# Optimization experiments

Measured on AMD Instinct MI355X. Metric: run time of the kernel, lower is better.

Reference implementation:

```python
import jax, jax.numpy as jnp
import numpy as np

N = 50_000       # nodes
E = 1_600_000    # edges per edge set (avg degree 32)
D = 128          # hidden dim
F_IN = 1273      # fixed num_features in NetGIN
G = 512          # graphs in batch
STEPS = 6        # Set2Set processing steps
BN_EPS = 1e-5


def setup_inputs() -> dict:
    key = jax.random.key(0)
    ks = iter(jax.random.split(key, 40))
    def rn(shape, fan_in):
        return jax.random.normal(next(ks), shape, jnp.float32) / np.float32(np.sqrt(fan_in))
    inp = {}
    inp["x"] = jax.random.normal(next(ks), (N, F_IN), jnp.float32)
    for i in (1, 2, 3):
        inp[f"edge_index_{i}"] = jax.random.randint(next(ks), (2, E), 0, N, jnp.int32)
    inp["batch"] = jnp.sort(jax.random.randint(next(ks), (N,), 0, G, jnp.int32))
    # GINConv MLPs: layer 1 has input F_IN, layers 2-6 have input D
    inp["conv1_W1"] = rn((3, F_IN, D), F_IN)
    inp["conv1_b1"] = jnp.zeros((3, D), jnp.float32)
    inp["conv_rest_W1"] = rn((5, 3, D, D), D)
    inp["conv_rest_b1"] = jnp.zeros((5, 3, D), jnp.float32)
    inp["conv_W2"] = rn((6, 3, D, D), D)
    inp["conv_b2"] = jnp.zeros((6, 3, D), jnp.float32)
    inp["conv_bn1_g"] = jnp.ones((6, 3, D), jnp.float32)
    inp["conv_bn1_b"] = jnp.zeros((6, 3, D), jnp.float32)
    inp["conv_bn2_g"] = jnp.ones((6, 3, D), jnp.float32)
    inp["conv_bn2_b"] = jnp.zeros((6, 3, D), jnp.float32)
    inp["conv_eps"] = jnp.zeros((6, 3), jnp.float32)  # train_eps=True, init 0
    # fusion MLPs (3*D -> D -> D)
    inp["mlp_W1"] = rn((6, 3 * D, D), 3 * D)
    inp["mlp_b1"] = jnp.zeros((6, D), jnp.float32)
    inp["mlp_bn1_g"] = jnp.ones((6, D), jnp.float32)
    inp["mlp_bn1_b"] = jnp.zeros((6, D), jnp.float32)
    inp["mlp_W2"] = rn((6, D, D), D)
    inp["mlp_b2"] = jnp.zeros((6, D), jnp.float32)
    inp["mlp_bn2_g"] = jnp.ones((6, D), jnp.float32)
    inp["mlp_bn2_b"] = jnp.zeros((6, D), jnp.float32)
    # Set2Set single-layer LSTM: input 2D, hidden D; gate order i,f,g,o
    inp["lstm_Wih"] = rn((4 * D, 2 * D), 2 * D)
    inp["lstm_Whh"] = rn((4 * D, D), D)
    inp["lstm_bih"] = jnp.zeros((4 * D,), jnp.float32)
    inp["lstm_bhh"] = jnp.zeros((4 * D,), jnp.float32)
    inp["fc1_W"] = rn((2 * D, D), 2 * D)
    inp["fc1_b"] = jnp.zeros((D,), jnp.float32)
    inp["fc4_W"] = rn((D, 12), D)
    inp["fc4_b"] = jnp.zeros((12,), jnp.float32)
    return inp


def _bn(x, g, b):
    # BatchNorm1d in training mode: batch statistics (biased var), eps=1e-5
    mu = jnp.mean(x, axis=0)
    var = jnp.var(x, axis=0)
    return g * (x - mu) * jax.lax.rsqrt(var + BN_EPS) + b


def _mlp2(h, W1, b1, g1, bb1, W2, b2, g2, bb2):
    h = jax.nn.relu(_bn(h @ W1 + b1, g1, bb1))
    return jax.nn.relu(_bn(h @ W2 + b2, g2, bb2))


def _gin(h, ei, eps, W1, b1, g1, bb1, W2, b2, g2, bb2):
    # sum-aggregate neighbor features: out[dst] += h[src]
    agg = jax.ops.segment_sum(h[ei[0]], ei[1], num_segments=h.shape[0])
    return _mlp2((1.0 + eps) * h + agg, W1, b1, g1, bb1, W2, b2, g2, bb2)


def _forward(x, conv1_W1, conv1_b1, conv_rest_W1, conv_rest_b1, conv_W2, conv_b2,
             conv_bn1_g, conv_bn1_b, conv_bn2_g, conv_bn2_b, conv_eps,
             mlp_W1, mlp_b1, mlp_bn1_g, mlp_bn1_b, mlp_W2, mlp_b2, mlp_bn2_g, mlp_bn2_b,
             lstm_Wih, lstm_Whh, lstm_bih, lstm_bhh, fc1_W, fc1_b, fc4_W, fc4_b,
             edge_index_1, edge_index_2, edge_index_3, batch):
    edges = (edge_index_1, edge_index_2, edge_index_3)
    h = x
    for l in range(6):
        xs = []
        for k in range(3):
            W1 = conv1_W1[k] if l == 0 else conv_rest_W1[l - 1, k]
            b1 = conv1_b1[k] if l == 0 else conv_rest_b1[l - 1, k]
            xk = jax.nn.relu(_gin(h, edges[k], conv_eps[l, k], W1, b1,
                                  conv_bn1_g[l, k], conv_bn1_b[l, k],
                                  conv_W2[l, k], conv_b2[l, k],
                                  conv_bn2_g[l, k], conv_bn2_b[l, k]))
            xs.append(xk)
        h = _mlp2(jnp.concatenate(xs, axis=-1),
                  mlp_W1[l], mlp_b1[l], mlp_bn1_g[l], mlp_bn1_b[l],
                  mlp_W2[l], mlp_b2[l], mlp_bn2_g[l], mlp_bn2_b[l])
    # Set2Set readout (processing_steps=6)
    q_star = jnp.zeros((G, 2 * D), h.dtype)
    hh = jnp.zeros((G, D), h.dtype)
    cc = jnp.zeros((G, D), h.dtype)
    for _ in range(STEPS):
        gates = q_star @ lstm_Wih.T + hh @ lstm_Whh.T + lstm_bih + lstm_bhh
        i_g, f_g, g_g, o_g = jnp.split(gates, 4, axis=-1)
        cc = jax.nn.sigmoid(f_g) * cc + jax.nn.sigmoid(i_g) * jnp.tanh(g_g)
        hh = jax.nn.sigmoid(o_g) * jnp.tanh(cc)
        q = hh
        e = jnp.sum(h * q[batch], axis=-1)              # [N]
        emax = jax.ops.segment_max(e, batch, num_segments=G)
        ex = jnp.exp(e - emax[batch])
        denom = jax.ops.segment_sum(ex, batch, num_segments=G)
        a = ex / denom[batch]                            # per-graph softmax
        r = jax.ops.segment_sum(a[:, None] * h, batch, num_segments=G)
        q_star = jnp.concatenate([q, r], axis=-1)
    out = jax.nn.relu(q_star @ fc1_W + fc1_b)
    return out @ fc4_W + fc4_b                           # [G, 12]


def reference(x, conv1_W1, conv1_b1, conv_rest_W1, conv_rest_b1, conv_W2, conv_b2,
              conv_bn1_g, conv_bn1_b, conv_bn2_g, conv_bn2_b, conv_eps,
              mlp_W1, mlp_b1, mlp_bn1_g, mlp_bn1_b, mlp_W2, mlp_b2, mlp_bn2_g, mlp_bn2_b,
              lstm_Wih, lstm_Whh, lstm_bih, lstm_bhh, fc1_W, fc1_b, fc4_W, fc4_b,
              edge_index_1, edge_index_2, edge_index_3, batch):
    return _forward(x, conv1_W1, conv1_b1, conv_rest_W1, conv_rest_b1, conv_W2, conv_b2,
                    conv_bn1_g, conv_bn1_b, conv_bn2_g, conv_bn2_b, conv_eps,
                    mlp_W1, mlp_b1, mlp_bn1_g, mlp_bn1_b, mlp_W2, mlp_b2, mlp_bn2_g, mlp_bn2_b,
                    lstm_Wih, lstm_Whh, lstm_bih, lstm_bhh, fc1_W, fc1_b, fc4_W, fc4_b,
                    edge_index_1, edge_index_2, edge_index_3, batch)
```

## Files before the change

### kernel.cpp

```cpp
#include <hip/hip_runtime.h>
#include <cstdint>
#include <cstddef>

#define NN 50000
#define EE 1600000
#define GG 512
#define FIN 1273

typedef unsigned short u16;
typedef unsigned int u32;
typedef __attribute__((ext_vector_type(8))) short short8;
typedef __attribute__((ext_vector_type(4))) float f32x4;

__device__ __forceinline__ float sigmf(float x) { return 1.f / (1.f + expf(-x)); }

__device__ __forceinline__ void splitbf(float v, u16& hi, u16& lo) {
    const u32 u = __float_as_uint(v);
    hi = (u16)(u >> 16);
    const float rem = v - __uint_as_float(u & 0xffff0000u);
    lo = (u16)(__float_as_uint(rem) >> 16);
}

__device__ __forceinline__ void gload_lds16(const void* g, void* l) {
    __builtin_amdgcn_global_load_lds(
        (const __attribute__((address_space(1))) void*)g,
        (__attribute__((address_space(3))) void*)l, 16, 0, 0);
}

__device__ __forceinline__ bool remap3(int f, int nRow, int& mat, int& rt) {
    const int g = f / 24, w = f - g * 24;
    rt = g * 8 + (w & 7);
    mat = w >> 3;
    return rt < nRow;
}

__global__ __launch_bounds__(256) void gemm_l0(
    const float* __restrict__ A, int lda, int K, int Kreal,
    const u16* __restrict__ Bhi, const u16* __restrict__ Blo, size_t strideB,
    float* __restrict__ C, int ldc, int coffStep, int M, int nRow)
{
    __shared__ u16 lsAhi[128 * 64];
    __shared__ u16 lsAlo[128 * 64];
    __shared__ u16 lsBhi[128 * 64];
    __shared__ u16 lsBlo[128 * 64];
    int mat, rt;
    if (!remap3(blockIdx.x, nRow, mat, rt)) return;
    const int tid = threadIdx.x;
    const int wave = tid >> 6, lane = tid & 63;
    const int row0 = rt * 128;
    const int coff = mat * coffStep;
    const u16* Bh = Bhi + (size_t)mat * strideB;
    const u16* Bl = Blo + (size_t)mat * strideB;
    const int wm = wave >> 1, wn = wave & 1;
    f32x4 acc[4][4] = {};

    for (int k0 = 0; k0 < K; k0 += 64) {
        if (k0) __syncthreads();
        #pragma unroll
        for (int i = 0; i < 4; ++i) {
            const int slot = i * 256 + tid;
            const int r = slot >> 3, ch = tid & 7;
            int gr = row0 + r; if (gr >= M) gr = M - 1;
            const int kb = k0 + ch * 8;
            u16 th[8], tl[8];
            const float* src = A + (size_t)gr * lda + kb;
            if (kb + 8 <= Kreal) {
                const float4 v0 = *(const float4*)(src);
                const float4 v1 = *(const float4*)(src + 4);
                const float va[8] = {v0.x, v0.y, v0.z, v0.w,
                                     v1.x, v1.y, v1.z, v1.w};
                #pragma unroll
                for (int e = 0; e < 8; ++e) splitbf(va[e], th[e], tl[e]);
            } else {
                #pragma unroll
                for (int e = 0; e < 8; ++e) {
                    const float v = (kb + e < Kreal) ? src[e] : 0.f;
                    splitbf(v, th[e], tl[e]);
                }
            }
            const int off = (r << 6) + ((ch ^ (r & 7)) << 3);
            *(short8*)&lsAhi[off] = *(const short8*)th;
            *(short8*)&lsAlo[off] = *(const short8*)tl;
        }
        #pragma unroll
        for (int i = 0; i < 4; ++i) {
            const int slot = i * 256 + wave * 64 + lane;
            const int r = slot >> 3, ch = slot & 7;
            const int sch = ch ^ (r & 7);
            const size_t goff = (size_t)r * K + k0 + sch * 8;
            const int lbase = (i * 256 + wave * 64) * 8;
            gload_lds16(Bh + goff, &lsBhi[lbase]);
            gload_lds16(Bl + goff, &lsBlo[lbase]);
        }
        __syncthreads();
        #pragma unroll
        for (int ks = 0; ks < 2; ++ks) {
            short8 ah[4], al[4], bh[4], bl[4];
            const int kch = ks * 4 + (lane >> 4);
            #pragma unroll
            for (int m = 0; m < 4; ++m) {
                const int r = wm * 64 + m * 16 + (lane & 15);
                const int off = (r << 6) + ((kch ^ (r & 7)) << 3);
                ah[m] = *(const short8*)&lsAhi[off];
                al[m] = *(const short8*)&lsAlo[off];
            }
            #pragma unroll
            for (int n = 0; n < 4; ++n) {
                const int c = wn * 64 + n * 16 + (lane & 15);
                const int off = (c << 6) + ((kch ^ (c & 7)) << 3);
                bh[n] = *(const short8*)&lsBhi[off];
                bl[n] = *(const short8*)&lsBlo[off];
            }
            #pragma unroll
            for (int m = 0; m < 4; ++m)
                #pragma unroll
                for (int n = 0; n < 4; ++n) {
                    acc[m][n] = __builtin_amdgcn_mfma_f32_16x16x32_bf16(
                        ah[m], bh[n], acc[m][n], 0, 0, 0);
                    acc[m][n] = __builtin_amdgcn_mfma_f32_16x16x32_bf16(
                        ah[m], bl[n], acc[m][n], 0, 0, 0);
                    acc[m][n] = __builtin_amdgcn_mfma_f32_16x16x32_bf16(
                        al[m], bh[n], acc[m][n], 0, 0, 0);
                }
        }
    }
    #pragma unroll
    for (int n = 0; n < 4; ++n) {
        const int c = wn * 64 + n * 16 + (lane & 15);
        #pragma unroll
        for (int m = 0; m < 4; ++m) {
            #pragma unroll
            for (int j = 0; j < 4; ++j) {
                const int gr = row0 + wm * 64 + m * 16 + ((lane >> 4) << 2) + j;
                if (gr < M)
                    C[(size_t)gr * ldc + coff + c] = acc[m][n][j];
            }
        }
    }
}

template <int ABN>
__global__ __launch_bounds__(256) void gemm_dir(
    const float* __restrict__ A, size_t strideA, int lda, int K,
    const float* __restrict__ st, int stSlice, int stMat,
    const float* __restrict__ ga, const float* __restrict__ be,
    int gbSlice, int gbMat,
    const u16* __restrict__ Bhi, const u16* __restrict__ Blo, size_t strideB,
    const float* __restrict__ bias, int biasMat,
    float* __restrict__ C, int ldc, int coffStep,
    int M, int do_stats, float* __restrict__ stats_out, int ostatMat,
    int nMat, int nRow)
{
    __shared__ u16 lsBhi[128 * 64];
    __shared__ u16 lsBlo[128 * 64];
    int mat, rt;
    if (nMat == 3) {
        if (!remap3(blockIdx.x, nRow, mat, rt)) return;
    } else { mat = 0; rt = blockIdx.x; }
    const int tid = threadIdx.x;
    const int wave = tid >> 6, lane = tid & 63;
    const int row0 = rt * 128;
    const int wm = wave >> 1, wn = wave & 1;
    A += (size_t)mat * strideA;
    if (ABN) { st += mat * stMat; ga += mat * gbMat; be += mat * gbMat; }
    if (bias) bias += mat * biasMat;
    if (do_stats) stats_out += mat * ostatMat;
    const u16* Bh = Bhi + (size_t)mat * strideB;
    const u16* Bl = Blo + (size_t)mat * strideB;
    const int coff = mat * coffStep;
    f32x4 acc[4][4] = {};

    int arow[4];
    #pragma unroll
    for (int m = 0; m < 4; ++m) {
        int r = row0 + wm * 64 + m * 16 + (lane & 15);
        if (r >= M) r = M - 1;
        arow[m] = r;
    }

    for (int k0 = 0; k0 < K; k0 += 64) {
        if (k0) __syncthreads();
        #pragma unroll
        for (int i = 0; i < 4; ++i) {
            const int slot = i * 256 + wave * 64 + lane;
            const int r = slot >> 3, ch = slot & 7;
            const int sch = ch ^ (r & 7);
            const size_t goff = (size_t)r * K + k0 + sch * 8;
            const int lbase = (i * 256 + wave * 64) * 8;
            gload_lds16(Bh + goff, &lsBhi[lbase]);
            gload_lds16(Bl + goff, &lsBlo[lbase]);
        }
        __syncthreads();
        #pragma unroll
        for (int ks = 0; ks < 2; ++ks) {
            const int kch = ks * 4 + (lane >> 4);
            const int kb = k0 + kch * 8;
            float scv[8], shv[8];
            if (ABN) {
                const int s = kb >> 7, d0 = kb & 127;
                const float* stS = st + s * stSlice;
                const float* gS  = ga + s * gbSlice;
                const float* beS = be + s * gbSlice;
                #pragma unroll
                for (int e = 0; e < 8; ++e) {
                    const int d = d0 + e;
                    const float mu = stS[d] * (1.f / NN);
                    const float var = fmaxf(stS[128 + d] * (1.f / NN) - mu * mu, 0.f);
                    const float sc = gS[d] * rsqrtf(var + 1e-5f);
                    scv[e] = sc;
                    shv[e] = beS[d] - sc * mu;
                }
            }
            short8 ah[4], al[4];
            #pragma unroll
            for (int m = 0; m < 4; ++m) {
                const float* src = A + (size_t)arow[m] * lda + kb;
                const float4 v0 = *(const float4*)(src);
                const float4 v1 = *(const float4*)(src + 4);
                const float va[8] = {v0.x, v0.y, v0.z, v0.w,
                                     v1.x, v1.y, v1.z, v1.w};
                u16 th[8], tl[8];
                #pragma unroll
                for (int e = 0; e < 8; ++e) {
                    const float y = ABN
                        ? fmaxf(fmaf(scv[e], va[e], shv[e]), 0.f) : va[e];
                    splitbf(y, th[e], tl[e]);
                }
                ah[m] = *(const short8*)th;
                al[m] = *(const short8*)tl;
            }
            #pragma unroll
            for (int n = 0; n < 4; ++n) {
                const int c = wn * 64 + n * 16 + (lane & 15);
                const int off = (c << 6) + ((kch ^ (c & 7)) << 3);
                const short8 bh = *(const short8*)&lsBhi[off];
                const short8 bl = *(const short8*)&lsBlo[off];
                #pragma unroll
                for (int m = 0; m < 4; ++m) {
                    acc[m][n] = __builtin_amdgcn_mfma_f32_16x16x32_bf16(
                        ah[m], bh, acc[m][n], 0, 0, 0);
                    acc[m][n] = __builtin_amdgcn_mfma_f32_16x16x32_bf16(
                        ah[m], bl, acc[m][n], 0, 0, 0);
                    acc[m][n] = __builtin_amdgcn_mfma_f32_16x16x32_bf16(
                        al[m], bh, acc[m][n], 0, 0, 0);
                }
            }
        }
    }

    float colsum[4] = {0.f, 0.f, 0.f, 0.f}, colsq[4] = {0.f, 0.f, 0.f, 0.f};
    #pragma unroll
    for (int n = 0; n < 4; ++n) {
        const int c = wn * 64 + n * 16 + (lane & 15);
        const float bv = bias ? bias[c] : 0.f;
        #pragma unroll
        for (int m = 0; m < 4; ++m) {
            #pragma unroll
            for (int j = 0; j < 4; ++j) {
                const int gr = row0 + wm * 64 + m * 16 + ((lane >> 4) << 2) + j;
                if (gr < M) {
                    const float v = acc[m][n][j] + bv;
                    C[(size_t)gr * ldc + coff + c] = v;
                    colsum[n] += v; colsq[n] += v * v;
                }
            }
        }
    }
    if (do_stats) {
        float* ssum = (float*)lsBhi;
        float* ssq  = ssum + 128;
        __syncthreads();
        if (tid < 128) { ssum[tid] = 0.f; ssq[tid] = 0.f; }
        __syncthreads();
        #pragma unroll
        for (int n = 0; n < 4; ++n) {
            const int c = wn * 64 + n * 16 + (lane & 15);
            atomicAdd(&ssum[c], colsum[n]);
            atomicAdd(&ssq[c], colsq[n]);
        }
        __syncthreads();
        if (tid < 128) {
            atomicAdd(&stats_out[tid],       ssum[tid]);
            atomicAdd(&stats_out[128 + tid], ssq[tid]);
        }
    }
}

__global__ __launch_bounds__(256) void wt_cast2(const float* __restrict__ W,
                                                u16* __restrict__ Whi,
                                                u16* __restrict__ Wlo,
                                                int total, int K, int Kpad) {
    const int idx = blockIdx.x * 256 + threadIdx.x;
    if (idx >= total) return;
    const int perm = 128 * Kpad;
    const int m = idx / perm, rem = idx - m * perm;
    const int n = rem / Kpad, k = rem - n * Kpad;
    const float v = (k < K) ? W[(size_t)m * K * 128 + (size_t)k * 128 + n] : 0.f;
    u16 hi, lo;
    splitbf(v, hi, lo);
    Whi[idx] = hi; Wlo[idx] = lo;
}

template <bool BT>
__global__ __launch_bounds__(256) void gemm_f32(
    const float* __restrict__ A, const float* __restrict__ B,
    const float* __restrict__ bias, float* __restrict__ C,
    int M, int K, int Nc)
{
    __shared__ float As[32][68];
    __shared__ float Bs[32][132];
    const int tid = threadIdx.x;
    const int tx = tid & 15, ty = tid >> 4;
    const int row0 = blockIdx.x * 64, col0 = blockIdx.y * 128;
    float acc[4][8] = {};
    for (int k0 = 0; k0 < K; k0 += 32) {
        {
            const int kk = tid & 31, rb = tid >> 5;
            #pragma unroll
            for (int i = 0; i < 8; ++i) {
                const int r = rb + i * 8, gr = row0 + r, gk = k0 + kk;
                As[kk][r] = (gr < M && gk < K) ? A[(size_t)gr * K + gk] : 0.f;
            }
        }
        if (!BT) {
            const int c = tid & 127, kb = tid >> 7;
            #pragma unroll
            for (int i = 0; i < 16; ++i) {
                const int kk = kb + i * 2, gk = k0 + kk;
                Bs[kk][c] = (gk < K) ? B[(size_t)gk * Nc + col0 + c] : 0.f;
            }
        } else {
            const int kk = tid & 31, cb = tid >> 5;
            #pragma unroll
            for (int i = 0; i < 16; ++i) {
                const int c = cb + i * 8, gk = k0 + kk;
                Bs[kk][c] = (gk < K) ? B[(size_t)(col0 + c) * K + gk] : 0.f;
            }
        }
        __syncthreads();
        #pragma unroll 8
        for (int kk = 0; kk < 32; ++kk) {
            const float4 av  = *(const float4*)&As[kk][ty * 4];
            const float4 bv0 = *(const float4*)&Bs[kk][tx * 8];
            const float4 bv1 = *(const float4*)&Bs[kk][tx * 8 + 4];
            const float a[4] = {av.x, av.y, av.z, av.w};
            const float b[8] = {bv0.x, bv0.y, bv0.z, bv0.w, bv1.x, bv1.y, bv1.z, bv1.w};
            #pragma unroll
            for (int i = 0; i < 4; ++i)
                #pragma unroll
                for (int j = 0; j < 8; ++j)
                    acc[i][j] = fmaf(a[i], b[j], acc[i][j]);
        }
        __syncthreads();
    }
    #pragma unroll
    for (int j = 0; j < 8; ++j) {
        const float bv = bias ? bias[col0 + tx * 8 + j] : 0.f;
        #pragma unroll
        for (int i = 0; i < 4; ++i) acc[i][j] += bv;
    }
    #pragma unroll
    for (int i = 0; i < 4; ++i) {
        const int gr = row0 + ty * 4 + i;
        if (gr < M) {
            *(float4*)&C[(size_t)gr * Nc + col0 + tx * 8] =
                make_float4(acc[i][0], acc[i][1], acc[i][2], acc[i][3]);
            *(float4*)&C[(size_t)gr * Nc + col0 + tx * 8 + 4] =
                make_float4(acc[i][4], acc[i][5], acc[i][6], acc[i][7]);
        }
    }
}

__global__ __launch_bounds__(256) void count_deg(const int* __restrict__ dst,
                                                 int* __restrict__ deg) {
    const int e = blockIdx.x * 256 + threadIdx.x;
    if (e < EE) atomicAdd(&deg[dst[e]], 1);
}

__global__ __launch_bounds__(512) void scan1(const int* __restrict__ deg,
                                             int* __restrict__ scanned,
                                             int* __restrict__ bsum) {
    __shared__ int s[512];
    const int t = threadIdx.x;
    const int i = blockIdx.x * 512 + t;
    const int v = (i < NN) ? deg[i] : 0;
    s[t] = v; __syncthreads();
    for (int o = 1; o < 512; o <<= 1) {
        const int tv = (t >= o) ? s[t - o] : 0;
        __syncthreads();
        s[t] += tv;
        __syncthreads();
    }
    if (i < NN) scanned[i] = s[t];
    if (t == 511) bsum[blockIdx.x] = s[511];
}

__global__ __launch_bounds__(128) void scan2(int* __restrict__ bsum, int nb) {
    __shared__ int s[128];
    const int t = threadIdx.x;
    const int v = (t < nb) ? bsum[t] : 0;
    s[t] = v; __syncthreads();
    for (int o = 1; o < 128; o <<= 1) {
        const int tv = (t >= o) ? s[t - o] : 0;
        __syncthreads();
        s[t] += tv;
        __syncthreads();
    }
    if (t < nb) bsum[t] = s[t] - v;
}

__global__ __launch_bounds__(256) void scan3(const int* __restrict__ deg,
                                             const int* __restrict__ scanned,
                                             const int* __restrict__ bsum,
                                             int* __restrict__ rowptr,
                                             int* __restrict__ cursor) {
    const int i = blockIdx.x * 256 + threadIdx.x;
    if (i < NN) {
        const int v = bsum[i >> 9] + scanned[i] - deg[i];
        rowptr[i] = v; cursor[i] = v;
    }
    if (i == 0) rowptr[NN] = EE;
}

__global__ __launch_bounds__(256) void fill_csr(const int* __restrict__ src,
                                                const int* __restrict__ dst,
                                                int* __restrict__ cursor,
                                                int* __restrict__ csrc) {
    const int e = blockIdx.x * 256 + threadIdx.x;
    if (e < EE) {
        const int pos = atomicAdd(&cursor[dst[e]], 1);
        csrc[pos] = src[e];
    }
}

template <int L0>
__global__ __launch_bounds__(256) void agg_combine(
    const float* __restrict__ X, int ldp4,
    const int* __restrict__ rowptrB, const int* __restrict__ csrcB,
    const float* __restrict__ b1B,
    const float* __restrict__ stF2, const float* __restrict__ gam,
    const float* __restrict__ bet,
    const float* __restrict__ eps_arr, int epsBase,
    float* __restrict__ zB, float* __restrict__ statsB)
{
    __shared__ float red[256];
    const int k = blockIdx.y;
    const int* rowptr = rowptrB + (size_t)k * (NN + 1);
    const int* csrc   = csrcB + (size_t)k * EE;
    float* z          = zB + (size_t)k * NN * 128;
    const int tid = threadIdx.x, lane = tid & 63, wave = tid >> 6;
    const float e1 = 1.f + eps_arr[epsBase + k];
    const int half = lane >> 5;
    const int l32 = lane & 31;
    const float4* p4 = (const float4*)X + (L0 ? k * 32 : 0);
    float s[4] = {0.f, 0.f, 0.f, 0.f}, q[4] = {0.f, 0.f, 0.f, 0.f};
    float4 bv = make_float4(0.f, 0.f, 0.f, 0.f);
    float sc[4], sh[4];
    if (L0) {
        if (lane < 32) bv = ((const float4*)(b1B + k * 128))[l32];
    } else {
        #pragma unroll
        for (int c = 0; c < 4; ++c) {
            const int d = l32 * 4 + c;
            const float mu = stF2[d] * (1.f / NN);
            const float var = fmaxf(stF2[128 + d] * (1.f / NN) - mu * mu, 0.f);
            const float s_ = gam[d] * rsqrtf(var + 1e-5f);
            sc[c] = s_;
            sh[c] = bet[d] - s_ * mu;
        }
    }
    auto bnv = [&](float4 v) -> float4 {
        if (L0) return v;
        v.x = fmaxf(fmaf(sc[0], v.x, sh[0]), 0.f);
        v.y = fmaxf(fmaf(sc[1], v.y, sh[1]), 0.f);
        v.z = fmaxf(fmaf(sc[2], v.z, sh[2]), 0.f);
        v.w = fmaxf(fmaf(sc[3], v.w, sh[3]), 0.f);
        return v;
    };
    if (L0) { red[tid] = 0.f; __syncthreads(); }
    const int nbase = blockIdx.x * 16 + wave * 4;
    for (int t = 0; t < 4; ++t) {
        const int wid = nbase + t;
        const int s0 = rowptr[wid], s1 = rowptr[wid + 1];
        float ax = 0.f, ay = 0.f, az = 0.f, aw = 0.f;
        int j = s0;
        for (; j + 15 < s1; j += 16) {
            const int r0 = csrc[j + half],      r1 = csrc[j + 2 + half];
            const int r2 = csrc[j + 4 + half],  r3 = csrc[j + 6 + half];
            const int r4 = csrc[j + 8 + half],  r5 = csrc[j + 10 + half];
            const int r6 = csrc[j + 12 + half], r7 = csrc[j + 14 + half];
            const float4 v0 = bnv(p4[(size_t)r0 * ldp4 + l32]);
            const float4 v1 = bnv(p4[(size_t)r1 * ldp4 + l32]);
            const float4 v2 = bnv(p4[(size_t)r2 * ldp4 + l32]);
            const float4 v3 = bnv(p4[(size_t)r3 * ldp4 + l32]);
            const float4 v4 = bnv(p4[(size_t)r4 * ldp4 + l32]);
            const float4 v5 = bnv(p4[(size_t)r5 * ldp4 + l32]);
            const float4 v6 = bnv(p4[(size_t)r6 * ldp4 + l32]);
            const float4 v7 = bnv(p4[(size_t)r7 * ldp4 + l32]);
            ax += (v0.x + v1.x) + (v2.x + v3.x) + (v4.x + v5.x) + (v6.x + v7.x);
            ay += (v0.y + v1.y) + (v2.y + v3.y) + (v4.y + v5.y) + (v6.y + v7.y);
            az += (v0.z + v1.z) + (v2.z + v3.z) + (v4.z + v5.z) + (v6.z + v7.z);
            aw += (v0.w + v1.w) + (v2.w + v3.w) + (v4.w + v5.w) + (v6.w + v7.w);
        }
        for (; j + 7 < s1; j += 8) {
            const int r0 = csrc[j + half],     r1 = csrc[j + 2 + half];
            const int r2 = csrc[j + 4 + half], r3 = csrc[j + 6 + half];
            const float4 v0 = bnv(p4[(size_t)r0 * ldp4 + l32]);
            const float4 v1 = bnv(p4[(size_t)r1 * ldp4 + l32]);
            const float4 v2 = bnv(p4[(size_t)r2 * ldp4 + l32]);
            const float4 v3 = bnv(p4[(size_t)r3 * ldp4 + l32]);
            ax += (v0.x + v1.x) + (v2.x + v3.x);
            ay += (v0.y + v1.y) + (v2.y + v3.y);
            az += (v0.z + v1.z) + (v2.z + v3.z);
            aw += (v0.w + v1.w) + (v2.w + v3.w);
        }
        for (; j + 3 < s1; j += 4) {
            const float4 v0 = bnv(p4[(size_t)csrc[j + half] * ldp4 + l32]);
            const float4 v1 = bnv(p4[(size_t)csrc[j + 2 + half] * ldp4 + l32]);
            ax += v0.x + v1.x; ay += v0.y + v1.y;
            az += v0.z + v1.z; aw += v0.w + v1.w;
        }
        for (; j + 1 < s1; j += 2) {
            const float4 v0 = bnv(p4[(size_t)csrc[j + half] * ldp4 + l32]);
            ax += v0.x; ay += v0.y; az += v0.z; aw += v0.w;
        }
        if (j < s1 && half == 0) {
            const float4 v0 = bnv(p4[(size_t)csrc[j] * ldp4 + l32]);
            ax += v0.x; ay += v0.y; az += v0.z; aw += v0.w;
        }
        ax += __shfl_down(ax, 32, 64);
        ay += __shfl_down(ay, 32, 64);
        az += __shfl_down(az, 32, 64);
        aw += __shfl_down(aw, 32, 64);
        if (lane < 32) {
            const float4 self = bnv(p4[(size_t)wid * ldp4 + l32]);
            float4 zv;
            zv.x = fmaf(e1, self.x, ax + bv.x);
            zv.y = fmaf(e1, self.y, ay + bv.y);
            zv.z = fmaf(e1, self.z, az + bv.z);
            zv.w = fmaf(e1, self.w, aw + bv.w);
            ((float4*)z)[(size_t)wid * 32 + l32] = zv;
            if (L0) {
                s[0] += zv.x; s[1] += zv.y; s[2] += zv.z; s[3] += zv.w;
                q[0] += zv.x * zv.x; q[1] += zv.y * zv.y;
                q[2] += zv.z * zv.z; q[3] += zv.w * zv.w;
            }
        }
    }
    if (L0) {
        if (lane < 32) {
            const int d = l32 * 4;
            #pragma unroll
            for (int c = 0; c < 4; ++c) {
                atomicAdd(&red[d + c], s[c]);
                atomicAdd(&red[128 + d + c], q[c]);
            }
        }
        __syncthreads();
        atomicAdd(&statsB[(size_t)k * 512 + tid], red[tid]);
    }
}

__global__ __launch_bounds__(256) void bn_relu_f32(
    const float* __restrict__ xin, const float* __restrict__ stats,
    const float* __restrict__ gamma, const float* __restrict__ beta,
    float* __restrict__ out)
{
    const size_t i = (size_t)blockIdx.x * 256 + threadIdx.x;
    if (i >= (size_t)NN * 64) return;
    const int d = (int)(i & 63) * 2;
    const float inv_n = 1.f / NN;
    const float mu0 = stats[d] * inv_n,     mu1 = stats[d + 1] * inv_n;
    const float v0 = fmaxf(stats[128 + d] * inv_n - mu0 * mu0, 0.f);
    const float v1 = fmaxf(stats[129 + d] * inv_n - mu1 * mu1, 0.f);
    const float s0 = gamma[d] * rsqrtf(v0 + 1e-5f);
    const float s1 = gamma[d + 1] * rsqrtf(v1 + 1e-5f);
    const float2 xv = ((const float2*)xin)[i];
    const float y0 = fmaxf(fmaf(s0, xv.x - mu0, beta[d]), 0.f);
    const float y1 = fmaxf(fmaf(s1, xv.y - mu1, beta[d + 1]), 0.f);
    ((float2*)out)[i] = make_float2(y0, y1);
}

__global__ __launch_bounds__(256) void seg_starts(const int* __restrict__ batch,
                                                  int* __restrict__ gstart) {
    const int i = blockIdx.x * 256 + threadIdx.x;
    if (i >= NN) return;
    const int b = batch[i];
    if (i == 0) { for (int g = 0; g <= b; ++g) gstart[g] = 0; }
    else {
        const int pb = batch[i - 1];
        for (int g = pb + 1; g <= b; ++g) gstart[g] = i;
    }
    if (i == NN - 1) { for (int g = b + 1; g <= GG; ++g) gstart[g] = NN; }
}

__global__ __launch_bounds__(256) void pack_wcat(const float* __restrict__ Wih,
                                                 const float* __restrict__ Whh,
                                                 float* __restrict__ Wcat) {
    const int i = blockIdx.x * 256 + threadIdx.x;
    if (i >= 512 * 384) return;
    const int j = i / 384, k = i - j * 384;
    Wcat[i] = (k < 256) ? Wih[j * 256 + k] : Whh[j * 128 + (k - 256)];
}

__global__ __launch_bounds__(256) void lstm_kernel(
    const float* __restrict__ gates, const float* __restrict__ bih,
    const float* __restrict__ bhh, float* __restrict__ cc, float* __restrict__ S)
{
    const int i = blockIdx.x * 256 + threadIdx.x;
    if (i >= GG * 128) return;
    const int g = i >> 7, d = i & 127;
    const float* gr = gates + (size_t)g * 512;
    const float ig = gr[d]       + bih[d]       + bhh[d];
    const float fg = gr[128 + d] + bih[128 + d] + bhh[128 + d];
    const float gv = gr[256 + d] + bih[256 + d] + bhh[256 + d];
    const float og = gr[384 + d] + bih[384 + d] + bhh[384 + d];
    const float c  = sigmf(fg) * cc[i] + sigmf(ig) * tanhf(gv);
    const float hv = sigmf(og) * tanhf(c);
    cc[i] = c;
    S[(size_t)g * 384 + d] = hv;
    S[(size_t)g * 384 + 256 + d] = hv;
}

__global__ __launch_bounds__(256) void attend_kernel(
    const float* __restrict__ h, float* __restrict__ S,
    float* __restrict__ ews, const int* __restrict__ gstart)
{
    const int g = blockIdx.x;
    const int rs = gstart[g], re = gstart[g + 1];
    const int tid = threadIdx.x, lane = tid & 63, w = tid >> 6;
    __shared__ float q[128];
    __shared__ float red[8];
    if (tid < 128) q[tid] = S[(size_t)g * 384 + 256 + tid];
    __syncthreads();
    const float2* h2 = (const float2*)h;
    float lmax = -1e30f;
    for (int n = rs + w; n < re; n += 4) {
        const float2 hv = h2[(size_t)n * 64 + lane];
        float p = hv.x * q[2 * lane] + hv.y * q[2 * lane + 1];
        #pragma unroll
        for (int o = 32; o; o >>= 1) p += __shfl_down(p, o, 64);
        if (lane == 0) { ews[n] = p; lmax = fmaxf(lmax, p); }
    }
    if (lane == 0) red[w] = lmax;
    __syncthreads();
    const float m = fmaxf(fmaxf(red[0], red[1]), fmaxf(red[2], red[3]));
    __syncthreads();
    float lsum = 0.f;
    for (int n = rs + tid; n < re; n += 256) {
        const float ex = expf(ews[n] - m);
        ews[n] = ex; lsum += ex;
    }
    #pragma unroll
    for (int o = 32; o; o >>= 1) lsum += __shfl_down(lsum, o, 64);
    if (lane == 0) red[w] = lsum;
    __syncthreads();
    const float denom = red[0] + red[1] + red[2] + red[3];
    if (tid < 128) {
        float acc = 0.f;
        for (int n = rs; n < re; ++n)
            acc = fmaf(ews[n], h[(size_t)n * 128 + tid], acc);
        S[(size_t)g * 384 + 128 + tid] = (denom > 0.f) ? acc / denom : 0.f;
    }
}

__global__ __launch_bounds__(128) void fc1_kernel(const float* __restrict__ S,
                                                  const float* __restrict__ W,
                                                  const float* __restrict__ b,
                                                  float* __restrict__ out1) {
    const int g = blockIdx.x, d = threadIdx.x;
    __shared__ float qs[256];
    qs[d] = S[(size_t)g * 384 + d];
    qs[128 + d] = S[(size_t)g * 384 + 128 + d];
    __syncthreads();
    float acc = b[d];
    for (int k = 0; k < 256; ++k) acc = fmaf(qs[k], W[k * 128 + d], acc);
    out1[(size_t)g * 128 + d] = fmaxf(acc, 0.f);
}

__global__ __launch_bounds__(256) void fc4_kernel(const float* __restrict__ out1,
                                                  const float* __restrict__ W,
                                                  const float* __restrict__ b,
                                                  float* __restrict__ out) {
    const int i = blockIdx.x * 256 + threadIdx.x;
    if (i >= GG * 12) return;
    const int g = i / 12, j = i - g * 12;
    float acc = b[j];
    for (int d = 0; d < 128; ++d)
        acc = fmaf(out1[(size_t)g * 128 + d], W[d * 12 + j], acc);
    out[i] = acc;
}

extern "C" void kernel_launch(void* const* d_in, const int* in_sizes, int n_in,
                              void* d_out, int out_size, void* d_ws, size_t ws_size,
                              hipStream_t stream)
{
    const float* x        = (const float*)d_in[0];
    const int*   eidx[3]  = {(const int*)d_in[1], (const int*)d_in[2], (const int*)d_in[3]};
    const int*   batch    = (const int*)d_in[4];
    const float* conv1_W1     = (const float*)d_in[5];
    const float* conv1_b1     = (const float*)d_in[6];
    const float* conv_rest_W1 = (const float*)d_in[7];
    const float* conv_rest_b1 = (const float*)d_in[8];
    const float* conv_W2      = (const float*)d_in[9];
    const float* conv_b2      = (const float*)d_in[10];
    const float* conv_bn1_g   = (const float*)d_in[11];
    const float* conv_bn1_b   = (const float*)d_in[12];
    const float* conv_bn2_g   = (const float*)d_in[13];
    const float* conv_bn2_b   = (const float*)d_in[14];
    const float* conv_eps     = (const float*)d_in[15];
    const float* mlp_W1       = (const float*)d_in[16];
    const float* mlp_b1       = (const float*)d_in[17];
    const float* mlp_bn1_g    = (const float*)d_in[18];
    const float* mlp_bn1_b    = (const float*)d_in[19];
    const float* mlp_W2       = (const float*)d_in[20];
    const float* mlp_b2       = (const float*)d_in[21];
    const float* mlp_bn2_g    = (const float*)d_in[22];
    const float* mlp_bn2_b    = (const float*)d_in[23];
    const float* lstm_Wih     = (const float*)d_in[24];
    const float* lstm_Whh     = (const float*)d_in[25];
    const float* lstm_bih     = (const float*)d_in[26];
    const float* lstm_bhh     = (const float*)d_in[27];
    const float* fc1_W        = (const float*)d_in[28];
    const float* fc1_b        = (const float*)d_in[29];
    const float* fc4_W        = (const float*)d_in[30];
    const float* fc4_b        = (const float*)d_in[31];
    float* outp = (float*)d_out;

    float* f = (float*)d_ws;
    size_t fo = 0;
    float* X     = f + fo; fo += (size_t)NN * 384;
    float* sb    = f + fo; fo += (size_t)NN * 384;
    float* zm2   = f + fo; fo += (size_t)NN * 128;
    float* ews   = f + fo; fo += NN;
    float* stats = f + fo; fo += 48 * 256;
    float* S     = f + fo; fo += (size_t)GG * 384;
    float* ccb   = f + fo; fo += (size_t)GG * 128;
    float* gates = f + fo; fo += (size_t)GG * 512;
    float* Wcat  = f + fo; fo += (size_t)512 * 384;
    fo = (fo + 7) & ~(size_t)7;
    u16* b = (u16*)(f + fo);
    size_t bo = 0;
    u16* c1_hi   = b + bo; bo += (size_t)3 * 128 * 1280;
    u16* c1_lo   = b + bo; bo += (size_t)3 * 128 * 1280;
    u16* rw1_hi  = b + bo; bo += (size_t)15 * 128 * 128;
    u16* rw1_lo  = b + bo; bo += (size_t)15 * 128 * 128;
    u16* w2_hi   = b + bo; bo += (size_t)18 * 128 * 128;
    u16* w2_lo   = b + bo; bo += (size_t)18 * 128 * 128;
    u16* mw1_hi  = b + bo; bo += (size_t)6 * 128 * 384;
    u16* mw1_lo  = b + bo; bo += (size_t)6 * 128 * 384;
    u16* mw2_hi  = b + bo; bo += (size_t)6 * 128 * 128;
    u16* mw2_lo  = b + bo; bo += (size_t)6 * 128 * 128;
    int* ip = (int*)(b + bo);
    size_t io = 0;
    int* rowptr0 = ip + io; io += (size_t)3 * (NN + 1);
    int* csrc0   = ip + io; io += (size_t)3 * EE;
    int* deg     = ip + io; io += NN;
    int* cursor  = ip + io; io += NN;
    int* scanned = ip + io; io += NN;
    int* bsum    = ip + io; io += 128;
    int* gstart  = ip + io; io += GG + 1;
    const size_t need = fo * 4 + bo * 2 + io * 4;
    if (ws_size < need) return;

    const int NBLK_SCAN = (NN + 511) / 512;

    {
        int t;
        t = 3 * 128 * 1280;
        wt_cast2<<<(t + 255) / 256, 256, 0, stream>>>(conv1_W1, c1_hi, c1_lo, t, FIN, 1280);
        t = 15 * 128 * 128;
        wt_cast2<<<(t + 255) / 256, 256, 0, stream>>>(conv_rest_W1, rw1_hi, rw1_lo, t, 128, 128);
        t = 18 * 128 * 128;
        wt_cast2<<<(t + 255) / 256, 256, 0, stream>>>(conv_W2, w2_hi, w2_lo, t, 128, 128);
        t = 6 * 128 * 384;
        wt_cast2<<<(t + 255) / 256, 256, 0, stream>>>(mlp_W1, mw1_hi, mw1_lo, t, 384, 384);
        t = 6 * 128 * 128;
        wt_cast2<<<(t + 255) / 256, 256, 0, stream>>>(mlp_W2, mw2_hi, mw2_lo, t, 128, 128);
    }

    for (int s = 0; s < 3; ++s) {
        int* rowptr = rowptr0 + (size_t)s * (NN + 1);
        int* csrc   = csrc0 + (size_t)s * EE;
        hipMemsetAsync(deg, 0, NN * sizeof(int), stream);
        count_deg<<<(EE + 255) / 256, 256, 0, stream>>>(eidx[s] + EE, deg);
        scan1<<<NBLK_SCAN, 512, 0, stream>>>(deg, scanned, bsum);
        scan2<<<1, 128, 0, stream>>>(bsum, NBLK_SCAN);
        scan3<<<(NN + 255) / 256, 256, 0, stream>>>(deg, scanned, bsum, rowptr, cursor);
        fill_csr<<<(EE + 255) / 256, 256, 0, stream>>>(eidx[s], eidx[s] + EE, cursor, csrc);
    }
    seg_starts<<<(NN + 255) / 256, 256, 0, stream>>>(batch, gstart);
    hipMemsetAsync(stats, 0, 48 * 256 * sizeof(float), stream);
    hipMemsetAsync(S, 0, (size_t)GG * 384 * sizeof(float), stream);
    hipMemsetAsync(ccb, 0, (size_t)GG * 128 * sizeof(float), stream);

    const int G128 = (NN + 127) / 128;
    const int G3   = 24 * ((G128 + 7) / 8);
    const int AGG_GRID = NN / 16;

    for (int l = 0; l < 6; ++l) {
        float* stL    = stats + (size_t)l * 8 * 256;
        float* slotF1 = stL + 6 * 256;
        float* slotF2 = stL + 7 * 256;
        float* mlp1in  = (l == 0) ? X : sb;
        float* mlp1out = (l == 0) ? sb : X;

        if (l == 0) {
            gemm_l0<<<G3, 256, 0, stream>>>(
                x, FIN, 1280, FIN, c1_hi, c1_lo, (size_t)128 * 1280,
                X, 384, 128, NN, G128);
            agg_combine<1><<<dim3(AGG_GRID, 3), 256, 0, stream>>>(
                X, 96, rowptr0, csrc0, conv1_b1,
                nullptr, nullptr, nullptr, conv_eps, 0, sb, stL);
            gemm_dir<1><<<G3, 256, 0, stream>>>(
                sb, (size_t)NN * 128, 128, 128,
                stL, 0, 512,
                conv_bn1_g + l * 3 * 128, conv_bn1_b + l * 3 * 128, 0, 128,
                w2_hi + (size_t)l * 3 * 128 * 128,
                w2_lo + (size_t)l * 3 * 128 * 128, (size_t)128 * 128,
                conv_b2 + l * 3 * 128, 128,
                X, 384, 128, NN, 1, stL + 256, 512, 3, G128);
        } else {
            agg_combine<0><<<dim3(AGG_GRID, 3), 256, 0, stream>>>(
                zm2, 32, rowptr0, csrc0, nullptr,
                stats + (size_t)((l - 1) * 8 + 7) * 256,
                mlp_bn2_g + (l - 1) * 128, mlp_bn2_b + (l - 1) * 128,
                conv_eps, l * 3, sb, nullptr);
            gemm_dir<0><<<G3, 256, 0, stream>>>(
                sb, (size_t)NN * 128, 128, 128,
                nullptr, 0, 0, nullptr, nullptr, 0, 0,
                rw1_hi + (size_t)(l - 1) * 3 * 128 * 128,
                rw1_lo + (size_t)(l - 1) * 3 * 128 * 128, (size_t)128 * 128,
                conv_rest_b1 + (l - 1) * 3 * 128, 128,
                X, 384, 128, NN, 1, stL, 512, 3, G128);
            gemm_dir<1><<<G3, 256, 0, stream>>>(
                X, 128, 384, 128,
                stL, 0, 512,
                conv_bn1_g + l * 3 * 128, conv_bn1_b + l * 3 * 128, 0, 128,
                w2_hi + (size_t)l * 3 * 128 * 128,
                w2_lo + (size_t)l * 3 * 128 * 128, (size_t)128 * 128,
                conv_b2 + l * 3 * 128, 128,
                sb, 384, 128, NN, 1, stL + 256, 512, 3, G128);
        }

        gemm_dir<1><<<G128, 256, 0, stream>>>(
            mlp1in, 0, 384, 384,
            stL + 256, 512, 0,
            conv_bn2_g + l * 3 * 128, conv_bn2_b + l * 3 * 128, 128, 0,
            mw1_hi + (size_t)l * 128 * 384, mw1_lo + (size_t)l * 128 * 384, 0,
            mlp_b1 + l * 128, 0, mlp1out, 128, 0, NN, 1, slotF1, 0, 1, G128);

        gemm_dir<1><<<G128, 256, 0, stream>>>(
            mlp1out, 0, 128, 128,
            slotF1, 0, 0,
            mlp_bn1_g + l * 128, mlp_bn1_b + l * 128, 0, 0,
            mw2_hi + (size_t)l * 128 * 128, mw2_lo + (size_t)l * 128 * 128, 0,
            mlp_b2 + l * 128, 0, zm2, 128, 0, NN, 1, slotF2, 0, 1, G128);
    }
    bn_relu_f32<<<(NN * 64 + 255) / 256, 256, 0, stream>>>(
        zm2, stats + (size_t)(5 * 8 + 7) * 256,
        mlp_bn2_g + 5 * 128, mlp_bn2_b + 5 * 128, X);

    pack_wcat<<<(512 * 384 + 255) / 256, 256, 0, stream>>>(lstm_Wih, lstm_Whh, Wcat);
    for (int t = 0; t < 6; ++t) {
        gemm_f32<true><<<dim3(8, 4), 256, 0, stream>>>(
            S, Wcat, nullptr, gates, GG, 384, 512);
        lstm_kernel<<<(GG * 128 + 255) / 256, 256, 0, stream>>>(
            gates, lstm_bih, lstm_bhh, ccb, S);
        attend_kernel<<<GG, 256, 0, stream>>>(X, S, ews, gstart);
    }
    fc1_kernel<<<GG, 128, 0, stream>>>(S, fc1_W, fc1_b, gates);
    fc4_kernel<<<(GG * 12 + 255) / 256, 256, 0, stream>>>(gates, fc4_W, fc4_b, outp);
}
```

Baseline: 5.021 ms.

## Bucket CSR neighbors by source range and aggregate bucket-by-bucket for locality

Builds the CSR with each destination's neighbor list split into 13 buckets by source index (src>>12). Per-bucket offsets come from a second count array, and the aggregation kernel walks all nodes of a wave bucket by bucket. The goal is to keep gathered feature rows within a narrow source range at any moment so they hit L2 more often. In exchange, CSR construction needs extra atomics and a 13x larger offset array, and the aggregation inner loop loses its deep unrolling, so fewer loads are in flight per bucket.

```diff
diff --git a/kernel.cpp b/kernel.cpp
--- a/kernel.cpp
+++ b/kernel.cpp
@@ -6,6 +6,9 @@
 #define EE 1600000
 #define GG 512
 #define FIN 1273
+#define NB 13
+#define NBP1 14
+#define BSHIFT 12
 
 typedef unsigned short u16;
 typedef unsigned int u32;
@@ -371,10 +374,16 @@
     }
 }
 
-__global__ __launch_bounds__(256) void count_deg(const int* __restrict__ dst,
-                                                 int* __restrict__ deg) {
+__global__ __launch_bounds__(256) void count_both(const int* __restrict__ src,
+                                                  const int* __restrict__ dst,
+                                                  int* __restrict__ deg,
+                                                  int* __restrict__ cnt) {
     const int e = blockIdx.x * 256 + threadIdx.x;
-    if (e < EE) atomicAdd(&deg[dst[e]], 1);
+    if (e < EE) {
+        const int d = dst[e];
+        atomicAdd(&deg[d], 1);
+        atomicAdd(&cnt[d * NB + (src[e] >> BSHIFT)], 1);
+    }
 }
 
 __global__ __launch_bounds__(512) void scan1(const int* __restrict__ deg,
@@ -409,34 +418,40 @@
     if (t < nb) bsum[t] = s[t] - v;
 }
 
-__global__ __launch_bounds__(256) void scan3(const int* __restrict__ deg,
-                                             const int* __restrict__ scanned,
-                                             const int* __restrict__ bsum,
-                                             int* __restrict__ rowptr,
-                                             int* __restrict__ cursor) {
-    const int i = blockIdx.x * 256 + threadIdx.x;
-    if (i < NN) {
-        const int v = bsum[i >> 9] + scanned[i] - deg[i];
-        rowptr[i] = v; cursor[i] = v;
-    }
-    if (i == 0) rowptr[NN] = EE;
-}
-
-__global__ __launch_bounds__(256) void fill_csr(const int* __restrict__ src,
-                                                const int* __restrict__ dst,
-                                                int* __restrict__ cursor,
-                                                int* __restrict__ csrc) {
+__global__ __launch_bounds__(256) void mk_boff(const int* __restrict__ deg,
+                                               const int* __restrict__ scanned,
+                                               const int* __restrict__ bsum,
+                                               const int* __restrict__ cnt,
+                                               int* __restrict__ boff,
+                                               int* __restrict__ cursorB) {
+    const int d = blockIdx.x * 256 + threadIdx.x;
+    if (d >= NN) return;
+    int base = bsum[d >> 9] + scanned[d] - deg[d];
+    #pragma unroll
+    for (int b = 0; b < NB; ++b) {
+        boff[(size_t)d * NBP1 + b] = base;
+        cursorB[(size_t)d * NB + b] = base;
+        base += cnt[(size_t)d * NB + b];
+    }
+    boff[(size_t)d * NBP1 + NB] = base;
+}
+
+__global__ __launch_bounds__(256) void fillB(const int* __restrict__ src,
+                                             const int* __restrict__ dst,
+                                             int* __restrict__ cursorB,
+                                             int* __restrict__ csrc) {
     const int e = blockIdx.x * 256 + threadIdx.x;
     if (e < EE) {
-        const int pos = atomicAdd(&cursor[dst[e]], 1);
-        csrc[pos] = src[e];
+        const int s = src[e];
+        const int pos = atomicAdd(&cursorB[(size_t)dst[e] * NB + (s >> BSHIFT)], 1);
+        csrc[pos] = s;
     }
 }
 
 template <int L0>
 __global__ __launch_bounds__(256) void agg_combine(
     const float* __restrict__ X, int ldp4,
-    const int* __restrict__ rowptrB, const int* __restrict__ csrcB,
+    const int* __restrict__ boffB, const int* __restrict__ csrcB,
     const float* __restrict__ b1B,
     const float* __restrict__ stF2, const float* __restrict__ gam,
     const float* __restrict__ bet,
@@ -445,15 +460,14 @@
 {
     __shared__ float red[256];
     const int k = blockIdx.y;
-    const int* rowptr = rowptrB + (size_t)k * (NN + 1);
-    const int* csrc   = csrcB + (size_t)k * EE;
-    float* z          = zB + (size_t)k * NN * 128;
+    const int* boff = boffB + (size_t)k * NN * NBP1;
+    const int* csrc = csrcB + (size_t)k * EE;
+    float* z        = zB + (size_t)k * NN * 128;
     const int tid = threadIdx.x, lane = tid & 63, wave = tid >> 6;
     const float e1 = 1.f + eps_arr[epsBase + k];
     const int half = lane >> 5;
     const int l32 = lane & 31;
     const float4* p4 = (const float4*)X + (L0 ? k * 32 : 0);
-    float s[4] = {0.f, 0.f, 0.f, 0.f}, q[4] = {0.f, 0.f, 0.f, 0.f};
     float4 bv = make_float4(0.f, 0.f, 0.f, 0.f);
     float sc[4], sh[4];
     if (L0) {
@@ -479,55 +493,44 @@
     };
     if (L0) { red[tid] = 0.f; __syncthreads(); }
     const int nbase = blockIdx.x * 16 + wave * 4;
+
+    float ac[4][4] = {};
+    int prevOff[4];
+    #pragma unroll
+    for (int t = 0; t < 4; ++t)
+        prevOff[t] = boff[(size_t)(nbase + t) * NBP1];
+
+    for (int b = 0; b < NB; ++b) {
+        #pragma unroll
+        for (int t = 0; t < 4; ++t) {
+            const int s0 = prevOff[t];
+            const int s1 = boff[(size_t)(nbase + t) * NBP1 + b + 1];
+            prevOff[t] = s1;
+            float ax = 0.f, ay = 0.f, az = 0.f, aw = 0.f;
+            int j = s0;
+            for (; j + 3 < s1; j += 4) {
+                const float4 v0 = bnv(p4[(size_t)csrc[j + half] * ldp4 + l32]);
+                const float4 v1 = bnv(p4[(size_t)csrc[j + 2 + half] * ldp4 + l32]);
+                ax += v0.x + v1.x; ay += v0.y + v1.y;
+                az += v0.z + v1.z; aw += v0.w + v1.w;
+            }
+            for (; j + 1 < s1; j += 2) {
+                const float4 v0 = bnv(p4[(size_t)csrc[j + half] * ldp4 + l32]);
+                ax += v0.x; ay += v0.y; az += v0.z; aw += v0.w;
+            }
+            if (j < s1 && half == 0) {
+                const float4 v0 = bnv(p4[(size_t)csrc[j] * ldp4 + l32]);
+                ax += v0.x; ay += v0.y; az += v0.z; aw += v0.w;
+            }
+            ac[t][0] += ax; ac[t][1] += ay; ac[t][2] += az; ac[t][3] += aw;
+        }
+    }
+
+    float s_[4] = {0.f, 0.f, 0.f, 0.f}, q_[4] = {0.f, 0.f, 0.f, 0.f};
+    #pragma unroll
     for (int t = 0; t < 4; ++t) {
         const int wid = nbase + t;
-        const int s0 = rowptr[wid], s1 = rowptr[wid + 1];
-        float ax = 0.f, ay = 0.f, az = 0.f, aw = 0.f;
-        int j = s0;
-        for (; j + 15 < s1; j += 16) {
-            const int r0 = csrc[j + half],      r1 = csrc[j + 2 + half];
-            const int r2 = csrc[j + 4 + half],  r3 = csrc[j + 6 + half];
-            const int r4 = csrc[j + 8 + half],  r5 = csrc[j + 10 + half];
-            const int r6 = csrc[j + 12 + half], r7 = csrc[j + 14 + half];
-            const float4 v0 = bnv(p4[(size_t)r0 * ldp4 + l32]);
-            const float4 v1 = bnv(p4[(size_t)r1 * ldp4 + l32]);
-            const float4 v2 = bnv(p4[(size_t)r2 * ldp4 + l32]);
-            const float4 v3 = bnv(p4[(size_t)r3 * ldp4 + l32]);
-            const float4 v4 = bnv(p4[(size_t)r4 * ldp4 + l32]);
-            const float4 v5 = bnv(p4[(size_t)r5 * ldp4 + l32]);
-            const float4 v6 = bnv(p4[(size_t)r6 * ldp4 + l32]);
-            const float4 v7 = bnv(p4[(size_t)r7 * ldp4 + l32]);
-            ax += (v0.x + v1.x) + (v2.x + v3.x) + (v4.x + v5.x) + (v6.x + v7.x);
-            ay += (v0.y + v1.y) + (v2.y + v3.y) + (v4.y + v5.y) + (v6.y + v7.y);
-            az += (v0.z + v1.z) + (v2.z + v3.z) + (v4.z + v5.z) + (v6.z + v7.z);
-            aw += (v0.w + v1.w) + (v2.w + v3.w) + (v4.w + v5.w) + (v6.w + v7.w);
-        }
-        for (; j + 7 < s1; j += 8) {
-            const int r0 = csrc[j + half],     r1 = csrc[j + 2 + half];
-            const int r2 = csrc[j + 4 + half], r3 = csrc[j + 6 + half];
-            const float4 v0 = bnv(p4[(size_t)r0 * ldp4 + l32]);
-            const float4 v1 = bnv(p4[(size_t)r1 * ldp4 + l32]);
-            const float4 v2 = bnv(p4[(size_t)r2 * ldp4 + l32]);
-            const float4 v3 = bnv(p4[(size_t)r3 * ldp4 + l32]);
-            ax += (v0.x + v1.x) + (v2.x + v3.x);
-            ay += (v0.y + v1.y) + (v2.y + v3.y);
-            az += (v0.z + v1.z) + (v2.z + v3.z);
-            aw += (v0.w + v1.w) + (v2.w + v3.w);
-        }
-        for (; j + 3 < s1; j += 4) {
-            const float4 v0 = bnv(p4[(size_t)csrc[j + half] * ldp4 + l32]);
-            const float4 v1 = bnv(p4[(size_t)csrc[j + 2 + half] * ldp4 + l32]);
-            ax += v0.x + v1.x; ay += v0.y + v1.y;
-            az += v0.z + v1.z; aw += v0.w + v1.w;
-        }
-        for (; j + 1 < s1; j += 2) {
-            const float4 v0 = bnv(p4[(size_t)csrc[j + half] * ldp4 + l32]);
-            ax += v0.x; ay += v0.y; az += v0.z; aw += v0.w;
-        }
-        if (j < s1 && half == 0) {
-            const float4 v0 = bnv(p4[(size_t)csrc[j] * ldp4 + l32]);
-            ax += v0.x; ay += v0.y; az += v0.z; aw += v0.w;
-        }
+        float ax = ac[t][0], ay = ac[t][1], az = ac[t][2], aw = ac[t][3];
         ax += __shfl_down(ax, 32, 64);
         ay += __shfl_down(ay, 32, 64);
         az += __shfl_down(az, 32, 64);
@@ -541,9 +544,9 @@
             zv.w = fmaf(e1, self.w, aw + bv.w);
             ((float4*)z)[(size_t)wid * 32 + l32] = zv;
             if (L0) {
-                s[0] += zv.x; s[1] += zv.y; s[2] += zv.z; s[3] += zv.w;
-                q[0] += zv.x * zv.x; q[1] += zv.y * zv.y;
-                q[2] += zv.z * zv.z; q[3] += zv.w * zv.w;
+                s_[0] += zv.x; s_[1] += zv.y; s_[2] += zv.z; s_[3] += zv.w;
+                q_[0] += zv.x * zv.x; q_[1] += zv.y * zv.y;
+                q_[2] += zv.z * zv.z; q_[3] += zv.w * zv.w;
             }
         }
     }
@@ -552,8 +555,8 @@
             const int d = l32 * 4;
             #pragma unroll
             for (int c = 0; c < 4; ++c) {
-                atomicAdd(&red[d + c], s[c]);
-                atomicAdd(&red[128 + d + c], q[c]);
+                atomicAdd(&red[d + c], s_[c]);
+                atomicAdd(&red[128 + d + c], q_[c]);
             }
         }
         __syncthreads();
@@ -753,15 +756,17 @@
     u16* mw2_lo  = b + bo; bo += (size_t)6 * 128 * 128;
     int* ip = (int*)(b + bo);
     size_t io = 0;
-    int* rowptr0 = ip + io; io += (size_t)3 * (NN + 1);
+    int* boff0   = ip + io; io += (size_t)3 * NN * NBP1;
     int* csrc0   = ip + io; io += (size_t)3 * EE;
     int* deg     = ip + io; io += NN;
-    int* cursor  = ip + io; io += NN;
     int* scanned = ip + io; io += NN;
     int* bsum    = ip + io; io += 128;
     int* gstart  = ip + io; io += GG + 1;
     const size_t need = fo * 4 + bo * 2 + io * 4;
     if (ws_size < need) return;
+
+    int* cnt     = (int*)sb;
+    int* cursorB = (int*)sb + (size_t)NN * NB;
 
     const int NBLK_SCAN = (NN + 511) / 512;
 
@@ -780,14 +785,15 @@
     }
 
     for (int s = 0; s < 3; ++s) {
-        int* rowptr = rowptr0 + (size_t)s * (NN + 1);
-        int* csrc   = csrc0 + (size_t)s * EE;
+        int* boff = boff0 + (size_t)s * NN * NBP1;
+        int* csrc = csrc0 + (size_t)s * EE;
         hipMemsetAsync(deg, 0, NN * sizeof(int), stream);
-        count_deg<<<(EE + 255) / 256, 256, 0, stream>>>(eidx[s] + EE, deg);
+        hipMemsetAsync(cnt, 0, (size_t)NN * NB * sizeof(int), stream);
+        count_both<<<(EE + 255) / 256, 256, 0, stream>>>(eidx[s], eidx[s] + EE, deg, cnt);
         scan1<<<NBLK_SCAN, 512, 0, stream>>>(deg, scanned, bsum);
         scan2<<<1, 128, 0, stream>>>(bsum, NBLK_SCAN);
-        scan3<<<(NN + 255) / 256, 256, 0, stream>>>(deg, scanned, bsum, rowptr, cursor);
-        fill_csr<<<(EE + 255) / 256, 256, 0, stream>>>(eidx[s], eidx[s] + EE, cursor, csrc);
+        mk_boff<<<(NN + 255) / 256, 256, 0, stream>>>(deg, scanned, bsum, cnt, boff, cursorB);
+        fillB<<<(EE + 255) / 256, 256, 0, stream>>>(eidx[s], eidx[s] + EE, cursorB, csrc);
     }
     seg_starts<<<(NN + 255) / 256, 256, 0, stream>>>(batch, gstart);
     hipMemsetAsync(stats, 0, 48 * 256 * sizeof(float), stream);
@@ -810,7 +816,7 @@
                 x, FIN, 1280, FIN, c1_hi, c1_lo, (size_t)128 * 1280,
                 X, 384, 128, NN, G128);
             agg_combine<1><<<dim3(AGG_GRID, 3), 256, 0, stream>>>(
-                X, 96, rowptr0, csrc0, conv1_b1,
+                X, 96, boff0, csrc0, conv1_b1,
                 nullptr, nullptr, nullptr, conv_eps, 0, sb, stL);
             gemm_dir<1><<<G3, 256, 0, stream>>>(
                 sb, (size_t)NN * 128, 128, 128,
@@ -822,7 +828,7 @@
                 X, 384, 128, NN, 1, stL + 256, 512, 3, G128);
         } else {
             agg_combine<0><<<dim3(AGG_GRID, 3), 256, 0, stream>>>(
-                zm2, 32, rowptr0, csrc0, nullptr,
+                zm2, 32, boff0, csrc0, nullptr,
                 stats + (size_t)((l - 1) * 8 + 7) * 256,
                 mlp_bn2_g + (l - 1) * 128, mlp_bn2_b + (l - 1) * 128,
                 conv_eps, l * 3, sb, nullptr);
```

Result: slower. 6.066 ms (+20.8%).
